# Performance work log

Hardware: AMD Instinct MI355X
Metric: run time of the kernel (lower is better)

The kernel has to match this reference:

```python
import jax, jax.numpy as jnp
import numpy as np

D = 1024  # model_embedding_dim
T = 512   # n_future_dx
B = 16384


def setup_inputs() -> dict:
    key = jax.random.key(0)
    k1, k2, k3, k4, k5 = jax.random.split(key, 5)
    x = jax.random.normal(k1, (B, D), dtype=jnp.float32)
    # Linear layers: torch nn.Linear stores weight [out, in], bias [out]
    s = 1.0 / np.sqrt(D)
    Wh = jax.random.uniform(k2, (T, D), jnp.float32, -s, s)
    bh = jax.random.uniform(k3, (T,), jnp.float32, -s, s)
    Wb = jax.random.uniform(k4, (1, D), jnp.float32, -s, s)
    bb = jax.random.uniform(k5, (1,), jnp.float32, -s, s)
    return {"x": x, "Wh": Wh, "bh": bh, "Wb": Wb, "bb": bb}


def reference(x, Wh, bh, Wb, bb):
    # hazards = relu(x @ Wh^T + bh)  -> [B, T]
    hazards = jax.nn.relu(jnp.einsum('bd,td->bt', x, Wh) + bh)
    # masked expand-and-sum with upper-triangular mask (mask[i,j]=1 iff i<=j)
    # equals inclusive prefix sum along T.
    cum = jnp.cumsum(hazards, axis=1)
    base = jnp.einsum('bd,od->bo', x, Wb) + bb  # [B, 1]
    return cum + base
```

## Files before the change

### kernel.cpp

```cpp
#include <hip/hip_runtime.h>
#include <hip/hip_bf16.h>


typedef __bf16 bf16x8 __attribute__((ext_vector_type(8)));
typedef __bf16 bf16x4 __attribute__((ext_vector_type(4)));
typedef float f32x4 __attribute__((ext_vector_type(4)));

typedef const __attribute__((address_space(1))) void* gas_cptr;
typedef __attribute__((address_space(3))) void* las_ptr;

#define BM 64
#define BK 64
#define NKIT 16
#define TDIM 512
#define DDIM 1024
#define ASZ (BM * 128)
#define BSZ (TDIM * 128)

#define WAIT_TOP()  asm volatile("s_waitcnt vmcnt(6) lgkmcnt(0)" ::: "memory")
#define WAIT_LGKM() asm volatile("s_waitcnt lgkmcnt(0)" ::: "memory")
#define WAIT_VM0()  asm volatile("s_waitcnt vmcnt(0)" ::: "memory")
#define SBAR()      __builtin_amdgcn_s_barrier()

__global__ __launch_bounds__(256) void cvt_wh_kernel(const float* __restrict__ src,
                                                     __bf16* __restrict__ dst) {
    const int i = (blockIdx.x * 256 + threadIdx.x) * 4;
    const float4 v = *reinterpret_cast<const float4*>(src + i);
    bf16x4 o;
    o[0] = (__bf16)v.x; o[1] = (__bf16)v.y; o[2] = (__bf16)v.z; o[3] = (__bf16)v.w;
    *reinterpret_cast<bf16x4*>(dst + i) = o;
}

__device__ __forceinline__ int swz(int row) { return ((row >> 1) & 7) << 4; }

__global__ __launch_bounds__(1024, 4) void survival_kernel(
    const float* __restrict__ x,
    const __bf16* __restrict__ Whb,
    const float* __restrict__ bh,
    const float* __restrict__ Wb,
    const float* __restrict__ bbp,
    float* __restrict__ out)
{
    __shared__ __align__(16) char Alds[2][ASZ];
    __shared__ __align__(16) char Blds[2][BSZ];
    __shared__ float baseLds[BM];
    __shared__ float totLds[BM][8];

    const int tid  = threadIdx.x;
    const int lane = tid & 63;
    const int wid  = tid >> 6;
    const int wm   = wid >> 3;
    const int wn   = wid & 7;
    const int brow = blockIdx.x * BM;

    const float bb0 = bbp[0];

    const int ar = tid >> 4;
    const int ac = tid & 15;
    const float* xrow  = x  + (size_t)(brow + ar) * DDIM + ac * 4;
    const float* wbrow = Wb + ac * 4;
    char* const a_dst0 = &Alds[0][0] + ar * 128 + ((ac * 8) ^ swz(ar));

    const int b_row0 = wid * 32 + (lane >> 3);
    const int b_slot = lane & 7;

    float bpart = 0.f;
    f32x4 acc[2][4];
#pragma unroll
    for (int rt = 0; rt < 2; ++rt)
#pragma unroll
        for (int n = 0; n < 4; ++n)
            acc[rt][n] = (f32x4){0.f, 0.f, 0.f, 0.f};

    float4 xv, wv;

    auto stage_issue = [&](int buf, int it) {
        const int k0 = it * BK;
        xv = *reinterpret_cast<const float4*>(xrow + k0);
        wv = *reinterpret_cast<const float4*>(wbrow + k0);
#pragma unroll
        for (int c = 0; c < 4; ++c) {
            const int row  = b_row0 + c * 8;
            const int colb = (b_slot * 16) ^ swz(row);
            const __bf16* g = Whb + (size_t)row * DDIM + k0 + (colb >> 1);
            char* l = &Blds[0][0] + buf * BSZ + (wid * 32 + c * 8) * 128;
            __builtin_amdgcn_global_load_lds((gas_cptr)(const void*)g,
                                             (las_ptr)(void*)l, 16, 0, 0);
        }
    };

    auto stage_write = [&](int buf) {
        bpart += xv.x * wv.x + xv.y * wv.y + xv.z * wv.z + xv.w * wv.w;
        bf16x4 av;
        av[0] = (__bf16)xv.x; av[1] = (__bf16)xv.y;
        av[2] = (__bf16)xv.z; av[3] = (__bf16)xv.w;
        *reinterpret_cast<bf16x4*>(a_dst0 + buf * ASZ) = av;
    };

    auto compute = [&](int buf) {
        const char* Ab = &Alds[0][0] + buf * ASZ;
        const char* Bb = &Blds[0][0] + buf * BSZ;
#pragma unroll
        for (int h = 0; h < 2; ++h) {
            const int slot = (h * 4 + (lane >> 4)) * 16;
            bf16x8 af[2];
#pragma unroll
            for (int rt = 0; rt < 2; ++rt) {
                const int row = wm * 32 + rt * 16 + (lane & 15);
                af[rt] = *reinterpret_cast<const bf16x8*>(Ab + row * 128 + (slot ^ swz(row)));
            }
#pragma unroll
            for (int n = 0; n < 4; ++n) {
                const int trow = wn * 64 + n * 16 + (lane & 15);
                const bf16x8 bfr = *reinterpret_cast<const bf16x8*>(
                    Bb + trow * 128 + (slot ^ swz(trow)));
                acc[0][n] = __builtin_amdgcn_mfma_f32_16x16x32_bf16(af[0], bfr, acc[0][n], 0, 0, 0);
                acc[1][n] = __builtin_amdgcn_mfma_f32_16x16x32_bf16(af[1], bfr, acc[1][n], 0, 0, 0);
            }
        }
    };

    stage_issue(0, 0);
    stage_write(0);
    for (int it = 0; it < NKIT - 1; ++it) {
        const int cur = it & 1;
        const int nxt = cur ^ 1;
        stage_issue(nxt, it + 1);
        WAIT_TOP();
        SBAR();
        compute(cur);
        stage_write(nxt);
        WAIT_LGKM();
        SBAR();
    }
    WAIT_VM0();
    SBAR();
    compute((NKIT - 1) & 1);

    bpart += __shfl_xor(bpart, 1, 16);
    bpart += __shfl_xor(bpart, 2, 16);
    bpart += __shfl_xor(bpart, 4, 16);
    bpart += __shfl_xor(bpart, 8, 16);
    if ((tid & 15) == 0) baseLds[tid >> 4] = bpart + bb0;

    float bhv[4];
#pragma unroll
    for (int n = 0; n < 4; ++n)
        bhv[n] = bh[wn * 64 + n * 16 + (lane & 15)];

    float carry[2][4] = {{0.f,0.f,0.f,0.f},{0.f,0.f,0.f,0.f}};
#pragma unroll
    for (int n = 0; n < 4; ++n) {
#pragma unroll
        for (int rt = 0; rt < 2; ++rt) {
#pragma unroll
            for (int j = 0; j < 4; ++j) {
                float v = fmaxf(acc[rt][n][j] + bhv[n], 0.f);
#pragma unroll
                for (int off = 1; off < 16; off <<= 1) {
                    const float u = __shfl_up(v, (unsigned)off, 16);
                    if ((lane & 15) >= off) v += u;
                }
                v += carry[rt][j];
                carry[rt][j] = __shfl(v, 15, 16);
                acc[rt][n][j] = v;
            }
        }
    }

    if ((lane & 15) == 0) {
#pragma unroll
        for (int rt = 0; rt < 2; ++rt)
#pragma unroll
            for (int j = 0; j < 4; ++j) {
                const int r = wm * 32 + rt * 16 + (lane >> 4) * 4 + j;
                totLds[r][wn] = carry[rt][j];
            }
    }
    __syncthreads();

#pragma unroll
    for (int rt = 0; rt < 2; ++rt) {
#pragma unroll
        for (int j = 0; j < 4; ++j) {
            const int r = wm * 32 + rt * 16 + (lane >> 4) * 4 + j;
            float rc = baseLds[r];
#pragma unroll
            for (int w = 0; w < 7; ++w)
                if (w < wn) rc += totLds[r][w];
            float* orow = out + (size_t)(brow + r) * TDIM + wn * 64 + (lane & 15);
#pragma unroll
            for (int n = 0; n < 4; ++n)
                orow[n * 16] = acc[rt][n][j] + rc;
        }
    }
}

extern "C" void kernel_launch(void* const* d_in, const int* in_sizes, int n_in,
                              void* d_out, int out_size, void* d_ws, size_t ws_size,
                              hipStream_t stream) {
    const float* x  = (const float*)d_in[0];
    const float* Wh = (const float*)d_in[1];
    const float* bh = (const float*)d_in[2];
    const float* Wb = (const float*)d_in[3];
    const float* bb = (const float*)d_in[4];
    float* out = (float*)d_out;
    __bf16* Whb = (__bf16*)d_ws;

    cvt_wh_kernel<<<512, 256, 0, stream>>>(Wh, Whb);
    survival_kernel<<<256, 1024, 0, stream>>>(x, Whb, bh, Wb, bb, out);
}
```

Before: 134.6 us.

## Switch to triple-buffered pipeline with BK=32 and prefetch depth two

Halves the K tile to 32 and triple-buffers both the A and B shared-memory stages, so global loads run two iterations ahead of compute instead of one. The LDS swizzle and load mapping are rebuilt for 64-byte rows, and the x rows are loaded as float2 and packed into bf16 pairs. s_setprio is raised around the MFMA block. The aim is to hide global-load latency better, at the cost of twice as many barriers per block and less MFMA work between them.

Result: slower. 156.5 us (+16.3%).

```diff
diff --git a/kernel.cpp b/kernel.cpp
--- a/kernel.cpp
+++ b/kernel.cpp
@@ -10,17 +10,18 @@
 typedef __attribute__((address_space(3))) void* las_ptr;
 
 #define BM 64
-#define BK 64
-#define NKIT 16
+#define BK 32
+#define NKIT 32
 #define TDIM 512
 #define DDIM 1024
-#define ASZ (BM * 128)
-#define BSZ (TDIM * 128)
-
-#define WAIT_TOP()  asm volatile("s_waitcnt vmcnt(6) lgkmcnt(0)" ::: "memory")
+#define ABUF (BM * 64)
+#define BBUF (TDIM * 64)
+
+#define WAITV8()  asm volatile("s_waitcnt vmcnt(8) lgkmcnt(0)" ::: "memory")
+#define WAITV4()  asm volatile("s_waitcnt vmcnt(4) lgkmcnt(0)" ::: "memory")
+#define WAITV0()  asm volatile("s_waitcnt vmcnt(0) lgkmcnt(0)" ::: "memory")
 #define WAIT_LGKM() asm volatile("s_waitcnt lgkmcnt(0)" ::: "memory")
-#define WAIT_VM0()  asm volatile("s_waitcnt vmcnt(0)" ::: "memory")
-#define SBAR()      __builtin_amdgcn_s_barrier()
+#define SBAR()    __builtin_amdgcn_s_barrier()
 
 __global__ __launch_bounds__(256) void cvt_wh_kernel(const float* __restrict__ src,
                                                      __bf16* __restrict__ dst) {
@@ -31,7 +32,13 @@
     *reinterpret_cast<bf16x4*>(dst + i) = o;
 }
 
-__device__ __forceinline__ int swz(int row) { return ((row >> 1) & 7) << 4; }
+__device__ __forceinline__ int swz(int row) { return (row & 3) << 4; }
+
+__device__ __forceinline__ unsigned int pack_bf2(float a, float b) {
+    unsigned short lo = __builtin_bit_cast(unsigned short, (__bf16)a);
+    unsigned short hi = __builtin_bit_cast(unsigned short, (__bf16)b);
+    return ((unsigned int)hi << 16) | (unsigned int)lo;
+}
 
 __global__ __launch_bounds__(1024, 4) void survival_kernel(
     const float* __restrict__ x,
@@ -41,8 +48,8 @@
     const float* __restrict__ bbp,
     float* __restrict__ out)
 {
-    __shared__ __align__(16) char Alds[2][ASZ];
-    __shared__ __align__(16) char Blds[2][BSZ];
+    __shared__ __align__(16) char Alds[3][ABUF];
+    __shared__ __align__(16) char Blds[3][BBUF];
     __shared__ float baseLds[BM];
     __shared__ float totLds[BM][8];
 
@@ -51,18 +58,19 @@
     const int wid  = tid >> 6;
     const int wm   = wid >> 3;
     const int wn   = wid & 7;
+    const int tcol = lane & 15;
+    const int kq   = lane >> 4;
     const int brow = blockIdx.x * BM;
-
     const float bb0 = bbp[0];
 
     const int ar = tid >> 4;
-    const int ac = tid & 15;
-    const float* xrow  = x  + (size_t)(brow + ar) * DDIM + ac * 4;
-    const float* wbrow = Wb + ac * 4;
-    char* const a_dst0 = &Alds[0][0] + ar * 128 + ((ac * 8) ^ swz(ar));
-
-    const int b_row0 = wid * 32 + (lane >> 3);
-    const int b_slot = lane & 7;
+    const int ap = tid & 15;
+    const float* xrow = x + (size_t)(brow + ar) * DDIM + ap * 2;
+    const float* wbp  = Wb + ap * 2;
+    const int a_byte = ar * 64 + ((ap * 4) ^ swz(ar));
+
+    const int b_row0 = wid * 32 + (lane >> 2);
+    const int b_s    = lane & 3;
 
     float bpart = 0.f;
     f32x4 acc[2][4];
@@ -72,81 +80,81 @@
         for (int n = 0; n < 4; ++n)
             acc[rt][n] = (f32x4){0.f, 0.f, 0.f, 0.f};
 
-    float4 xv, wv;
-
-    auto stage_issue = [&](int buf, int it) {
+    float2 xr0, wr0, xr1, wr1;
+
+    auto issueT = [&](int buf, int it, int slot) {
         const int k0 = it * BK;
-        xv = *reinterpret_cast<const float4*>(xrow + k0);
-        wv = *reinterpret_cast<const float4*>(wbrow + k0);
-#pragma unroll
-        for (int c = 0; c < 4; ++c) {
-            const int row  = b_row0 + c * 8;
-            const int colb = (b_slot * 16) ^ swz(row);
-            const __bf16* g = Whb + (size_t)row * DDIM + k0 + (colb >> 1);
-            char* l = &Blds[0][0] + buf * BSZ + (wid * 32 + c * 8) * 128;
+        if (slot == 0) { xr0 = *reinterpret_cast<const float2*>(xrow + k0);
+                         wr0 = *reinterpret_cast<const float2*>(wbp + k0); }
+        else           { xr1 = *reinterpret_cast<const float2*>(xrow + k0);
+                         wr1 = *reinterpret_cast<const float2*>(wbp + k0); }
+#pragma unroll
+        for (int c = 0; c < 2; ++c) {
+            const int row = b_row0 + c * 16;
+            const int cb  = (b_s * 16) ^ swz(row);
+            const __bf16* g = Whb + (size_t)row * DDIM + k0 + (cb >> 1);
+            char* l = &Blds[buf][0] + (wid * 32 + c * 16) * 64;
             __builtin_amdgcn_global_load_lds((gas_cptr)(const void*)g,
                                              (las_ptr)(void*)l, 16, 0, 0);
         }
     };
 
-    auto stage_write = [&](int buf) {
-        bpart += xv.x * wv.x + xv.y * wv.y + xv.z * wv.z + xv.w * wv.w;
-        bf16x4 av;
-        av[0] = (__bf16)xv.x; av[1] = (__bf16)xv.y;
-        av[2] = (__bf16)xv.z; av[3] = (__bf16)xv.w;
-        *reinterpret_cast<bf16x4*>(a_dst0 + buf * ASZ) = av;
+    auto writeA = [&](int buf, int slot) {
+        const float2 xv = slot ? xr1 : xr0;
+        const float2 wv = slot ? wr1 : wr0;
+        bpart += xv.x * wv.x + xv.y * wv.y;
+        *reinterpret_cast<unsigned int*>(&Alds[buf][0] + a_byte) = pack_bf2(xv.x, xv.y);
     };
 
     auto compute = [&](int buf) {
-        const char* Ab = &Alds[0][0] + buf * ASZ;
-        const char* Bb = &Blds[0][0] + buf * BSZ;
-#pragma unroll
-        for (int h = 0; h < 2; ++h) {
-            const int slot = (h * 4 + (lane >> 4)) * 16;
-            bf16x8 af[2];
-#pragma unroll
-            for (int rt = 0; rt < 2; ++rt) {
-                const int row = wm * 32 + rt * 16 + (lane & 15);
-                af[rt] = *reinterpret_cast<const bf16x8*>(Ab + row * 128 + (slot ^ swz(row)));
-            }
-#pragma unroll
-            for (int n = 0; n < 4; ++n) {
-                const int trow = wn * 64 + n * 16 + (lane & 15);
-                const bf16x8 bfr = *reinterpret_cast<const bf16x8*>(
-                    Bb + trow * 128 + (slot ^ swz(trow)));
-                acc[0][n] = __builtin_amdgcn_mfma_f32_16x16x32_bf16(af[0], bfr, acc[0][n], 0, 0, 0);
-                acc[1][n] = __builtin_amdgcn_mfma_f32_16x16x32_bf16(af[1], bfr, acc[1][n], 0, 0, 0);
-            }
-        }
+        const char* Ab = &Alds[buf][0];
+        const char* Bb = &Blds[buf][0];
+        const int sl = kq * 16;
+        bf16x8 af[2];
+#pragma unroll
+        for (int rt = 0; rt < 2; ++rt) {
+            const int row = wm * 32 + rt * 16 + tcol;
+            af[rt] = *reinterpret_cast<const bf16x8*>(Ab + row * 64 + (sl ^ swz(row)));
+        }
+        __builtin_amdgcn_s_setprio(1);
+#pragma unroll
+        for (int n = 0; n < 4; ++n) {
+            const int trow = wn * 64 + n * 16 + tcol;
+            const bf16x8 bfr = *reinterpret_cast<const bf16x8*>(
+                Bb + trow * 64 + (sl ^ swz(trow)));
+            acc[0][n] = __builtin_amdgcn_mfma_f32_16x16x32_bf16(af[0], bfr, acc[0][n], 0, 0, 0);
+            acc[1][n] = __builtin_amdgcn_mfma_f32_16x16x32_bf16(af[1], bfr, acc[1][n], 0, 0, 0);
+        }
+        __builtin_amdgcn_s_setprio(0);
     };
 
-    stage_issue(0, 0);
-    stage_write(0);
-    for (int it = 0; it < NKIT - 1; ++it) {
-        const int cur = it & 1;
-        const int nxt = cur ^ 1;
-        stage_issue(nxt, it + 1);
-        WAIT_TOP();
+    issueT(0, 0, 0);
+    issueT(1, 1, 1);
+    writeA(0, 0);
+
+#pragma unroll
+    for (int t = 0; t < NKIT; ++t) {
+        if (t + 2 < NKIT) issueT((t + 2) % 3, t + 2, t & 1);
+        if (t + 2 < NKIT)      WAITV8();
+        else if (t + 1 < NKIT) WAITV4();
+        else                   WAITV0();
         SBAR();
-        compute(cur);
-        stage_write(nxt);
+        compute(t % 3);
+        if (t + 1 < NKIT) writeA((t + 1) % 3, (t + 1) & 1);
         WAIT_LGKM();
         SBAR();
     }
-    WAIT_VM0();
-    SBAR();
-    compute((NKIT - 1) & 1);
 
     bpart += __shfl_xor(bpart, 1, 16);
     bpart += __shfl_xor(bpart, 2, 16);
     bpart += __shfl_xor(bpart, 4, 16);
     bpart += __shfl_xor(bpart, 8, 16);
-    if ((tid & 15) == 0) baseLds[tid >> 4] = bpart + bb0;
+    if (ap == 0) baseLds[ar] = bpart + bb0;
 
     float bhv[4];
 #pragma unroll
     for (int n = 0; n < 4; ++n)
-        bhv[n] = bh[wn * 64 + n * 16 + (lane & 15)];
+        bhv[n] = bh[wn * 64 + n * 16 + tcol];
 
     float carry[2][4] = {{0.f,0.f,0.f,0.f},{0.f,0.f,0.f,0.f}};
 #pragma unroll
@@ -159,7 +167,7 @@
 #pragma unroll
                 for (int off = 1; off < 16; off <<= 1) {
                     const float u = __shfl_up(v, (unsigned)off, 16);
-                    if ((lane & 15) >= off) v += u;
+                    if (tcol >= off) v += u;
                 }
                 v += carry[rt][j];
                 carry[rt][j] = __shfl(v, 15, 16);
@@ -168,12 +176,12 @@
         }
     }
 
-    if ((lane & 15) == 0) {
+    if (tcol == 0) {
 #pragma unroll
         for (int rt = 0; rt < 2; ++rt)
 #pragma unroll
             for (int j = 0; j < 4; ++j) {
-                const int r = wm * 32 + rt * 16 + (lane >> 4) * 4 + j;
+                const int r = wm * 32 + rt * 16 + kq * 4 + j;
                 totLds[r][wn] = carry[rt][j];
             }
     }
@@ -183,12 +191,12 @@
     for (int rt = 0; rt < 2; ++rt) {
 #pragma unroll
         for (int j = 0; j < 4; ++j) {
-            const int r = wm * 32 + rt * 16 + (lane >> 4) * 4 + j;
+            const int r = wm * 32 + rt * 16 + kq * 4 + j;
             float rc = baseLds[r];
 #pragma unroll
             for (int w = 0; w < 7; ++w)
                 if (w < wn) rc += totLds[r][w];
-            float* orow = out + (size_t)(brow + r) * TDIM + wn * 64 + (lane & 15);
+            float* orow = out + (size_t)(brow + r) * TDIM + wn * 64 + tcol;
 #pragma unroll
             for (int n = 0; n < 4; ++n)
                 orow[n * 16] = acc[rt][n][j] + rc;
```
